# Kernel tuning notes

Hardware: AMD Instinct MI355X
Metric: run time of the kernel (lower is better)

## Reference

```python
import jax, jax.numpy as jnp
import numpy as np

EMBEDDING_DIM = 128
CODEBOOK_SIZE = 8192
COMMITMENT_COST = 0.25


def setup_inputs() -> dict:
    key = jax.random.key(0)
    k1, k2 = jax.random.split(key)
    inputs = jax.random.normal(k1, (8, 2048, EMBEDDING_DIM), dtype=jnp.float32)
    embeddings = jax.random.normal(k2, (EMBEDDING_DIM, CODEBOOK_SIZE), dtype=jnp.float32)
    return {"inputs": inputs, "embeddings": embeddings}


def reference(inputs, embeddings):
    # inputs: [B, T, D]; embeddings: [D, K]
    B, T, D = inputs.shape
    K = embeddings.shape[1]
    flat = inputs.reshape(-1, D)                      # [N, D]
    sim = flat @ embeddings                           # [N, K]
    dists = (jnp.sum(flat * flat, axis=1, keepdims=True)
             - 2.0 * sim
             + jnp.sum(embeddings * embeddings, axis=0, keepdims=True))
    idx_flat = jnp.argmax(-dists, axis=1)             # [N], matches tf.argmax(-d)
    encodings = jax.nn.one_hot(idx_flat, K, dtype=inputs.dtype)  # [N, K]
    encoding_indices = idx_flat.reshape(B, T)
    quantized = jnp.take(embeddings.T, encoding_indices, axis=0)  # [B, T, D]
    e_latent_loss = jnp.mean((jax.lax.stop_gradient(quantized) - inputs) ** 2)
    q_latent_loss = jnp.mean((quantized - jax.lax.stop_gradient(inputs)) ** 2)
    loss = q_latent_loss + COMMITMENT_COST * e_latent_loss
    quantized = inputs + jax.lax.stop_gradient(quantized - inputs)  # straight-through
    return quantized, encodings, encoding_indices, loss
```

## Files before the change

kernel.cpp:

```cpp
#include <hip/hip_runtime.h>

#define D 128
#define K 8192
#define N 16384
#define BM 32
#define TILES 64
#define GRP 4
#define THREADS 256
#define CAND_CAP 1024
#define DELTA 0.5f
#define RMIN_INIT 0xFF800000u

typedef __attribute__((ext_vector_type(4))) float f32x4;
typedef __attribute__((ext_vector_type(16))) float f32x16;
typedef __attribute__((ext_vector_type(8))) short short8;

__device__ __forceinline__ unsigned short f2bf(float f) {
    unsigned int b = __float_as_uint(f);
    return (unsigned short)((b + 0x7FFFu + ((b >> 16) & 1u)) >> 16);
}
__device__ __forceinline__ unsigned int fsort(float f) {
    unsigned int b = __float_as_uint(f);
    return b ^ ((unsigned int)((int)b >> 31) | 0x80000000u);
}
__device__ __forceinline__ float funsort(unsigned int u) {
    return __uint_as_float((u & 0x80000000u) ? (u ^ 0x80000000u) : ~u);
}

__global__ __launch_bounds__(256) void prep_kernel(const float* __restrict__ E,
        unsigned short* __restrict__ e1t, float* __restrict__ e2t,
        float* __restrict__ enorm) {
    __shared__ float esum[8][32];
    const int t = threadIdx.x;
    const int kl = t & 31, dg = t >> 5;
    const int k = blockIdx.x * 32 + kl;
    float s = 0.f;
    __align__(16) unsigned short tmpb[16];
    __align__(16) float tmpf[16];
#pragma unroll
    for (int j = 0; j < 16; ++j) {
        float v = E[(size_t)(dg * 16 + j) * K + k];
        s += v * v;
        tmpb[j] = f2bf(v);
        tmpf[j] = v;
    }
    *(f32x4*)(e1t + (size_t)k * D + dg * 16) = *(const f32x4*)tmpb;
    *(f32x4*)(e1t + (size_t)k * D + dg * 16 + 8) = *(const f32x4*)(tmpb + 8);
    if (e2t) {
#pragma unroll
        for (int q = 0; q < 4; ++q)
            *(f32x4*)(e2t + (size_t)k * D + dg * 16 + 4 * q) = *(const f32x4*)(tmpf + 4 * q);
    }
    esum[dg][kl] = s;
    __syncthreads();
    if (t < 32) {
        float e = 0.f;
#pragma unroll
        for (int g = 0; g < 8; ++g) e += esum[g][t];
        enorm[blockIdx.x * 32 + t] = e;
    }
}

template<int E2T>
__global__ __launch_bounds__(THREADS, 2) void main_kernel(
        const float* __restrict__ X, const float* __restrict__ E,
        const unsigned short* __restrict__ e1t, const float* __restrict__ e2t,
        const float* __restrict__ enorm, float* __restrict__ out,
        float* __restrict__ partials) {
    __shared__ unsigned long long cand[CAND_CAP];
    __shared__ unsigned long long best[BM];
    __shared__ unsigned int rmin[BM];
    __shared__ float red[THREADS];
    __shared__ int candn;

    const int t = threadIdx.x;
    const int wid = t >> 6, l = t & 63;
    const int l31 = l & 31, lh = l >> 5;
    const int wn = wid;
    const int rowbase = blockIdx.x * BM;

    float* qout = out;
    float* enc = out + (size_t)N * D;
    float* idxout = enc + (size_t)N * K;
    float* stripe = enc + (size_t)rowbase * K;

    if (t < BM) { rmin[t] = RMIN_INIT; best[t] = ~0ull; }
    if (t == 0) candn = 0;
    __syncthreads();

    short8 afr[8];
    {
        const int row = rowbase + l31;
#pragma unroll
        for (int ks = 0; ks < 8; ++ks) {
            const float* xp = X + (size_t)row * D + ks * 16 + lh * 8;
            f32x4 v0 = *(const f32x4*)xp;
            f32x4 v1 = *(const f32x4*)(xp + 4);
            short8 a;
            a[0] = (short)f2bf(v0[0]); a[1] = (short)f2bf(v0[1]);
            a[2] = (short)f2bf(v0[2]); a[3] = (short)f2bf(v0[3]);
            a[4] = (short)f2bf(v1[0]); a[5] = (short)f2bf(v1[1]);
            a[6] = (short)f2bf(v1[2]); a[7] = (short)f2bf(v1[3]);
            afr[ks] = a;
        }
    }

    const f32x4 z = {0.f, 0.f, 0.f, 0.f};

    for (int cg = 0; cg < TILES / GRP; ++cg) {
        f32x16 dsv[GRP];
#pragma unroll
        for (int g = 0; g < GRP; ++g) {
            const int ti = cg * GRP + g;
            const int col0 = ti * 128 + wn * 32;
            const int c = col0 + l31;

            short8 bf[8];
            const unsigned short* bp = e1t + (size_t)c * D + lh * 8;
#pragma unroll
            for (int ks = 0; ks < 8; ++ks)
                bf[ks] = *(const short8*)(bp + ks * 16);
            const float en = enorm[c];
            asm volatile("" ::: "memory");

            {
                float* base = stripe + (size_t)ti * 4096;
#pragma unroll
                for (int j = 0; j < 4; ++j)
                    __builtin_nontemporal_store(z, (f32x4*)(base + j * 1024 + t * 4));
            }

#pragma unroll
            for (int r = 0; r < 16; ++r) dsv[g][r] = 0.f;
#pragma unroll
            for (int ks = 0; ks < 8; ++ks)
                dsv[g] = __builtin_amdgcn_mfma_f32_32x32x16_bf16(afr[ks], bf[ks], dsv[g], 0, 0, 0);
#pragma unroll
            for (int r = 0; r < 16; ++r)
                dsv[g][r] = fmaf(-2.f, dsv[g][r], en);
        }

        float lmin[16];
#pragma unroll
        for (int r = 0; r < 16; ++r)
            lmin[r] = fminf(fminf(dsv[0][r], dsv[1][r]),
                            fminf(dsv[2][r], dsv[3][r]));
#pragma unroll
        for (int m = 1; m <= 16; m <<= 1)
#pragma unroll
            for (int r = 0; r < 16; ++r)
                lmin[r] = fminf(lmin[r], __shfl_xor(lmin[r], m, 64));

        float thrv[16];
#pragma unroll
        for (int q = 0; q < 4; ++q) {
            const int base = 8 * q + 4 * lh;
            uint4 rv = *(const uint4*)&rmin[base];
            thrv[4 * q + 0] = funsort(rv.x);
            thrv[4 * q + 1] = funsort(rv.y);
            thrv[4 * q + 2] = funsort(rv.z);
            thrv[4 * q + 3] = funsort(rv.w);
        }

#pragma unroll
        for (int r = 0; r < 16; ++r) {
            const int ro = (r & 3) + 8 * (r >> 2) + 4 * lh;
            const float te = fminf(thrv[r], lmin[r]) + DELTA;
#pragma unroll
            for (int g = 0; g < GRP; ++g) {
                if (dsv[g][r] < te) {
                    const int col = (cg * GRP + g) * 128 + wn * 32 + l31;
                    int ci = atomicAdd(&candn, 1);
                    if (ci < CAND_CAP)
                        cand[ci] = ((unsigned long long)fsort(dsv[g][r]) << 32) |
                                   ((unsigned long long)ro << 13) | (unsigned)col;
                }
            }
            if (l31 == 0 && lmin[r] < thrv[r])
                atomicMin(&rmin[ro], fsort(lmin[r]));
        }
    }

    __syncthreads();

    {
        int n = candn; if (n > CAND_CAP) n = CAND_CAP;
        for (int i = wid; i < n; i += 4) {
            const unsigned long long e = cand[i];
            const float dta = funsort((unsigned int)(e >> 32));
            const int ro = (int)((e >> 13) & 63u);
            const int col = (int)(e & 8191u);
            if (dta < funsort(rmin[ro]) + DELTA) {
                const int row = rowbase + ro;
                float x0 = X[(size_t)row * D + l];
                float x1 = X[(size_t)row * D + 64 + l];
                float e0, e1;
                if (E2T) {
                    e0 = e2t[(size_t)col * D + l];
                    e1 = e2t[(size_t)col * D + 64 + l];
                } else {
                    e0 = E[(size_t)l * K + col];
                    e1 = E[(size_t)(l + 64) * K + col];
                }
                float s = x0 * e0 + x1 * e1;
#pragma unroll
                for (int m = 1; m <= 32; m <<= 1) s += __shfl_xor(s, m, 64);
                if (l == 0) {
                    float dtx = enorm[col] - 2.f * s;
                    atomicMin(&best[ro],
                        ((unsigned long long)fsort(dtx) << 32) | (unsigned)col);
                }
            }
        }
    }
    __syncthreads();

    if (t < BM) {
        const int k = (int)(best[t] & 8191ull);
        idxout[rowbase + t] = (float)k;
        __builtin_nontemporal_store(1.0f, &enc[(size_t)(rowbase + t) * K + k]);
    }

    const int rr = t >> 3, sL = t & 7;
    const int row = rowbase + rr;
    const int kb = (int)(best[rr] & 8191ull);
    float part = 0.f;
#pragma unroll
    for (int j = 0; j < 4; ++j) {
        const int d0 = sL * 16 + 4 * j;
        f32x4 xv = *(const f32x4*)(X + (size_t)row * D + d0);
        f32x4 ev;
        if (E2T) {
            ev = *(const f32x4*)(e2t + (size_t)kb * D + d0);
        } else {
#pragma unroll
            for (int u = 0; u < 4; ++u) ev[u] = E[(size_t)(d0 + u) * K + kb];
        }
        f32x4 qv;
#pragma unroll
        for (int u = 0; u < 4; ++u) {
            float df = ev[u] - xv[u];
            qv[u] = xv[u] + df;
            part += df * df;
        }
        *(f32x4*)(qout + (size_t)row * D + d0) = qv;
    }
    red[t] = part;
    __syncthreads();
#pragma unroll
    for (int off = THREADS / 2; off > 0; off >>= 1) {
        if (t < off) red[t] += red[t + off];
        __syncthreads();
    }
    if (t == 0) partials[blockIdx.x] = red[0];
}

__global__ __launch_bounds__(256) void loss_kernel(const float* __restrict__ partials,
                                                   float* __restrict__ out) {
    __shared__ float red[256];
    const int t = threadIdx.x;
    red[t] = partials[t] + partials[t + 256];
    __syncthreads();
    for (int off = 128; off > 0; off >>= 1) {
        if (t < off) red[t] += red[t + off];
        __syncthreads();
    }
    if (t == 0) {
        float mean = red[0] / (float)((size_t)N * D);
        out[(size_t)N * D + (size_t)N * K + N] = mean + 0.25f * mean;
    }
}

extern "C" void kernel_launch(void* const* d_in, const int* in_sizes, int n_in,
                              void* d_out, int out_size, void* d_ws, size_t ws_size,
                              hipStream_t stream) {
    const float* X = (const float*)d_in[0];
    const float* E = (const float*)d_in[1];
    float* out = (float*)d_out;
    char* ws = (char*)d_ws;

    const size_t E1T_B = (size_t)K * D * 2;
    const size_t E2T_B = (size_t)K * D * 4;
    const bool use_e2t = ws_size >= E1T_B + E2T_B + 64 * 1024;

    unsigned short* e1t = (unsigned short*)ws;
    float* e2t; float* enorm; float* partials;
    if (use_e2t) {
        e2t = (float*)(ws + E1T_B);
        enorm = (float*)(ws + E1T_B + E2T_B);
        partials = enorm + K;
    } else {
        e2t = nullptr;
        enorm = (float*)(ws + E1T_B);
        partials = enorm + K;
    }

    hipLaunchKernelGGL(prep_kernel, dim3(K / 32), dim3(256), 0, stream,
                       E, e1t, e2t, enorm);
    if (use_e2t)
        hipLaunchKernelGGL((main_kernel<1>), dim3(N / BM), dim3(THREADS), 0, stream,
                           X, E, e1t, e2t, enorm, out, partials);
    else
        hipLaunchKernelGGL((main_kernel<0>), dim3(N / BM), dim3(THREADS), 0, stream,
                           X, E, e1t, e2t, enorm, out, partials);
    hipLaunchKernelGGL(loss_kernel, dim3(1), dim3(256), 0, stream, partials, out);
}
```

Baseline: 193.2 us.

## Split one-hot zero fill across separate kernel and widen main kernel to 8 waves

Moves zeroing of the first 5120 columns of the one-hot encoding matrix into a separate fill kernel. The main kernel zeroes only the remaining columns, interleaved with its first 24 tiles. The main kernel now runs 512 threads (8 waves), each wave handling one 32-column slice of 256-column tiles. It keeps one accumulator per tile instead of four grouped ones, and tracks per-row minima with LDS atomics instead of shuffle reductions per group. This is meant to balance the heavy store bandwidth against the MFMA work and to raise occupancy. The cost is an extra launch, more per-candidate atomics, and a larger candidate buffer.

```diff
diff --git a/kernel.cpp b/kernel.cpp
--- a/kernel.cpp
+++ b/kernel.cpp
@@ -4,10 +4,10 @@
 #define K 8192
 #define N 16384
 #define BM 32
-#define TILES 64
-#define GRP 4
-#define THREADS 256
-#define CAND_CAP 1024
+#define TILES 32
+#define FCOLS 5120
+#define THREADS 512
+#define CAND_CAP 2048
 #define DELTA 0.5f
 #define RMIN_INIT 0xFF800000u
 
@@ -61,8 +61,21 @@
     }
 }
 
+__global__ __launch_bounds__(256) void fill_kernel(float* __restrict__ enc) {
+    const unsigned int u0 = blockIdx.x * 256 + threadIdx.x;
+    const unsigned int stride = 4096 * 256;
+    const f32x4 z = {0.f, 0.f, 0.f, 0.f};
+#pragma unroll
+    for (int i = 0; i < 20; ++i) {
+        unsigned int u = u0 + (unsigned int)i * stride;
+        unsigned int row = u / (FCOLS / 4);
+        unsigned int c4 = u % (FCOLS / 4);
+        *(f32x4*)(enc + (size_t)row * K + c4 * 4) = z;
+    }
+}
+
 template<int E2T>
-__global__ __launch_bounds__(THREADS, 2) void main_kernel(
+__global__ __launch_bounds__(THREADS, 4) void main_kernel(
         const float* __restrict__ X, const float* __restrict__ E,
         const unsigned short* __restrict__ e1t, const float* __restrict__ e2t,
         const float* __restrict__ enorm, float* __restrict__ out,
@@ -76,13 +89,11 @@
     const int t = threadIdx.x;
     const int wid = t >> 6, l = t & 63;
     const int l31 = l & 31, lh = l >> 5;
-    const int wn = wid;
     const int rowbase = blockIdx.x * BM;
 
     float* qout = out;
     float* enc = out + (size_t)N * D;
     float* idxout = enc + (size_t)N * K;
-    float* stripe = enc + (size_t)rowbase * K;
 
     if (t < BM) { rmin[t] = RMIN_INIT; best[t] = ~0ull; }
     if (t == 0) candn = 0;
@@ -106,78 +117,81 @@
     }
 
     const f32x4 z = {0.f, 0.f, 0.f, 0.f};
-
-    for (int cg = 0; cg < TILES / GRP; ++cg) {
-        f32x16 dsv[GRP];
-#pragma unroll
-        for (int g = 0; g < GRP; ++g) {
-            const int ti = cg * GRP + g;
-            const int col0 = ti * 128 + wn * 32;
-            const int c = col0 + l31;
-
-            short8 bf[8];
-            const unsigned short* bp = e1t + (size_t)c * D + lh * 8;
-#pragma unroll
-            for (int ks = 0; ks < 8; ++ks)
-                bf[ks] = *(const short8*)(bp + ks * 16);
-            const float en = enorm[c];
-            asm volatile("" ::: "memory");
-
-            {
-                float* base = stripe + (size_t)ti * 4096;
-#pragma unroll
-                for (int j = 0; j < 4; ++j)
-                    __builtin_nontemporal_store(z, (f32x4*)(base + j * 1024 + t * 4));
-            }
-
-#pragma unroll
-            for (int r = 0; r < 16; ++r) dsv[g][r] = 0.f;
-#pragma unroll
-            for (int ks = 0; ks < 8; ++ks)
-                dsv[g] = __builtin_amdgcn_mfma_f32_32x32x16_bf16(afr[ks], bf[ks], dsv[g], 0, 0, 0);
-#pragma unroll
-            for (int r = 0; r < 16; ++r)
-                dsv[g][r] = fmaf(-2.f, dsv[g][r], en);
-        }
-
-        float lmin[16];
+    float thrv[16];
+#pragma unroll
+    for (int r = 0; r < 16; ++r) thrv[r] = __uint_as_float(0x7F800000u);
+
+    for (int ti = 0; ti < TILES; ++ti) {
+        const int c = ti * 256 + wid * 32 + l31;
+
+        short8 bf[8];
+        const unsigned short* bp = e1t + (size_t)c * D + lh * 8;
+#pragma unroll
+        for (int ks = 0; ks < 8; ++ks)
+            bf[ks] = *(const short8*)(bp + ks * 16);
+        const float en = enorm[c];
+        asm volatile("" ::: "memory");
+
+        if (ti < 24) {
+#pragma unroll
+            for (int s = 0; s < 2; ++s) {
+                const int j = ti * 2 + s;
+                const int rl = j / 12, kb = j % 12;
+                __builtin_nontemporal_store(z,
+                    (f32x4*)(enc + (size_t)(rowbase + wid * 4 + rl) * K + FCOLS + kb * 256 + l * 4));
+            }
+        }
+
+        f32x16 acc;
+#pragma unroll
+        for (int r = 0; r < 16; ++r) acc[r] = 0.f;
+#pragma unroll
+        for (int ks = 0; ks < 8; ++ks)
+            acc = __builtin_amdgcn_mfma_f32_32x32x16_bf16(afr[ks], bf[ks], acc, 0, 0, 0);
 #pragma unroll
         for (int r = 0; r < 16; ++r)
-            lmin[r] = fminf(fminf(dsv[0][r], dsv[1][r]),
-                            fminf(dsv[2][r], dsv[3][r]));
-#pragma unroll
-        for (int m = 1; m <= 16; m <<= 1)
-#pragma unroll
-            for (int r = 0; r < 16; ++r)
-                lmin[r] = fminf(lmin[r], __shfl_xor(lmin[r], m, 64));
-
-        float thrv[16];
-#pragma unroll
-        for (int q = 0; q < 4; ++q) {
-            const int base = 8 * q + 4 * lh;
-            uint4 rv = *(const uint4*)&rmin[base];
-            thrv[4 * q + 0] = funsort(rv.x);
-            thrv[4 * q + 1] = funsort(rv.y);
-            thrv[4 * q + 2] = funsort(rv.z);
-            thrv[4 * q + 3] = funsort(rv.w);
-        }
-
-#pragma unroll
-        for (int r = 0; r < 16; ++r) {
-            const int ro = (r & 3) + 8 * (r >> 2) + 4 * lh;
-            const float te = fminf(thrv[r], lmin[r]) + DELTA;
-#pragma unroll
-            for (int g = 0; g < GRP; ++g) {
-                if (dsv[g][r] < te) {
-                    const int col = (cg * GRP + g) * 128 + wn * 32 + l31;
+            acc[r] = fmaf(-2.f, acc[r], en);
+
+        if (ti == 0) {
+#pragma unroll
+            for (int r = 0; r < 16; ++r) thrv[r] = acc[r];
+#pragma unroll
+            for (int m = 1; m <= 16; m <<= 1)
+#pragma unroll
+                for (int r = 0; r < 16; ++r)
+                    thrv[r] = fminf(thrv[r], __shfl_xor(thrv[r], m, 64));
+#pragma unroll
+            for (int r = 0; r < 16; ++r) {
+                const int ro = (r & 3) + 8 * (r >> 2) + 4 * lh;
+                if (acc[r] < thrv[r] + DELTA) {
                     int ci = atomicAdd(&candn, 1);
                     if (ci < CAND_CAP)
-                        cand[ci] = ((unsigned long long)fsort(dsv[g][r]) << 32) |
-                                   ((unsigned long long)ro << 13) | (unsigned)col;
+                        cand[ci] = ((unsigned long long)fsort(acc[r]) << 32) |
+                                   ((unsigned long long)ro << 13) | (unsigned)c;
                 }
-            }
-            if (l31 == 0 && lmin[r] < thrv[r])
-                atomicMin(&rmin[ro], fsort(lmin[r]));
+                if (l31 == 0) atomicMin(&rmin[ro], fsort(thrv[r]));
+            }
+        } else {
+#pragma unroll
+            for (int q = 0; q < 4; ++q) {
+                uint4 rv = *(const uint4*)&rmin[8 * q + 4 * lh];
+                thrv[4 * q + 0] = funsort(rv.x);
+                thrv[4 * q + 1] = funsort(rv.y);
+                thrv[4 * q + 2] = funsort(rv.z);
+                thrv[4 * q + 3] = funsort(rv.w);
+            }
+#pragma unroll
+            for (int r = 0; r < 16; ++r) {
+                const int ro = (r & 3) + 8 * (r >> 2) + 4 * lh;
+                if (acc[r] < thrv[r] + DELTA) {
+                    int ci = atomicAdd(&candn, 1);
+                    if (ci < CAND_CAP)
+                        cand[ci] = ((unsigned long long)fsort(acc[r]) << 32) |
+                                   ((unsigned long long)ro << 13) | (unsigned)c;
+                    if (acc[r] < thrv[r])
+                        atomicMin(&rmin[ro], fsort(acc[r]));
+                }
+            }
         }
     }
 
@@ -185,7 +199,7 @@
 
     {
         int n = candn; if (n > CAND_CAP) n = CAND_CAP;
-        for (int i = wid; i < n; i += 4) {
+        for (int i = wid; i < n; i += 8) {
             const unsigned long long e = cand[i];
             const float dta = funsort((unsigned int)(e >> 32));
             const int ro = (int)((e >> 13) & 63u);
@@ -218,16 +232,16 @@
     if (t < BM) {
         const int k = (int)(best[t] & 8191ull);
         idxout[rowbase + t] = (float)k;
-        __builtin_nontemporal_store(1.0f, &enc[(size_t)(rowbase + t) * K + k]);
-    }
-
-    const int rr = t >> 3, sL = t & 7;
+        enc[(size_t)(rowbase + t) * K + k] = 1.0f;
+    }
+
+    const int rr = t >> 4, sL = t & 15;
     const int row = rowbase + rr;
     const int kb = (int)(best[rr] & 8191ull);
     float part = 0.f;
 #pragma unroll
-    for (int j = 0; j < 4; ++j) {
-        const int d0 = sL * 16 + 4 * j;
+    for (int j = 0; j < 2; ++j) {
+        const int d0 = sL * 8 + 4 * j;
         f32x4 xv = *(const f32x4*)(X + (size_t)row * D + d0);
         f32x4 ev;
         if (E2T) {
@@ -277,6 +291,7 @@
     const float* X = (const float*)d_in[0];
     const float* E = (const float*)d_in[1];
     float* out = (float*)d_out;
+    float* enc = out + (size_t)N * D;
     char* ws = (char*)d_ws;
 
     const size_t E1T_B = (size_t)K * D * 2;
@@ -297,6 +312,7 @@
 
     hipLaunchKernelGGL(prep_kernel, dim3(K / 32), dim3(256), 0, stream,
                        E, e1t, e2t, enorm);
+    hipLaunchKernelGGL(fill_kernel, dim3(4096), dim3(256), 0, stream, enc);
     if (use_e2t)
         hipLaunchKernelGGL((main_kernel<1>), dim3(N / BM), dim3(THREADS), 0, stream,
                            X, E, e1t, e2t, enorm, out, partials);
```

After: 221.0 us. 14.4% more time.
